# Kernel tuning notes

Hardware: AMD Instinct MI355X
Metric: run time of the kernel (lower is better)

Reference implementation:

```python
import jax, jax.numpy as jnp
import numpy as np

B_, L_, D_MODEL = 2, 4096, 1024
D_STATE, D_CONV, D_INNER = 64, 4, 2048
EPS = 1.1920929e-07  # torch.finfo(float32).eps, nn.RMSNorm default


def setup_inputs() -> dict:
    key = jax.random.key(0)
    ks = jax.random.split(key, 8)
    s = 0.02
    x = jax.random.normal(ks[0], (B_, L_, D_MODEL), jnp.float32)
    W_in = jax.random.normal(ks[1], (D_MODEL, 2 * D_INNER), jnp.float32) * s
    conv_w = jax.random.normal(ks[2], (D_INNER, 1, D_CONV), jnp.float32) * s  # depthwise (O,I/g,K)
    conv_b = jnp.zeros((D_INNER,), jnp.float32)
    W_x = jax.random.normal(ks[3], (D_INNER, 2 * D_STATE + D_INNER), jnp.float32) * s
    W_dt = jax.random.normal(ks[4], (D_INNER, D_INNER), jnp.float32) * s
    b_dt = jnp.zeros((D_INNER,), jnp.float32)
    A_log = jnp.log(jnp.tile(jnp.arange(1, D_STATE + 1, dtype=jnp.float32)[None, :], (D_INNER, 1)))
    D_param = jnp.ones((D_INNER,), jnp.float32)
    W_out = jax.random.normal(ks[5], (D_INNER, D_MODEL), jnp.float32) * s
    norm_w = jnp.ones((D_INNER,), jnp.float32)
    return dict(x=x, W_in=W_in, conv_w=conv_w, conv_b=conv_b, W_x=W_x, W_dt=W_dt,
                b_dt=b_dt, A_log=A_log, D_param=D_param, W_out=W_out, norm_w=norm_w)


def selective_scan(x_conv, dt, A, B_ssm, C_ssm, D_param):
    # x_conv,dt: (B,L,d_inner); A:(d_inner,d_state); B_ssm,C_ssm:(B,L,d_state)
    dt = jax.nn.softplus(dt)

    def step(h, inp):
        dt_t, B_t, C_t, x_t = inp  # (B,di),(B,ds),(B,ds),(B,di)
        dA = jnp.exp(dt_t[:, :, None] * A[None, :, :])           # (B,di,ds)
        h = dA * h + (dt_t * x_t)[:, :, None] * B_t[:, None, :]  # (B,di,ds)
        y = jnp.einsum('bds,bs->bd', h, C_t)                     # (B,di)
        return h, y

    h0 = jnp.zeros((x_conv.shape[0], A.shape[0], A.shape[1]), x_conv.dtype)
    xs = (jnp.moveaxis(dt, 1, 0), jnp.moveaxis(B_ssm, 1, 0),
          jnp.moveaxis(C_ssm, 1, 0), jnp.moveaxis(x_conv, 1, 0))
    _, ys = jax.lax.scan(step, h0, xs)
    y = jnp.moveaxis(ys, 0, 1)  # (B,L,d_inner)
    return y + x_conv * D_param[None, None, :]


def reference(x, W_in, conv_w, conv_b, W_x, W_dt, b_dt, A_log, D_param, W_out, norm_w):
    xz = x @ W_in                                    # (B,L,2*d_inner)
    x_ssm, z = jnp.split(xz, 2, axis=-1)
    # causal depthwise conv1d: left-pad d_conv-1 == torch pad-both-then-slice[:L]
    xc = jnp.swapaxes(x_ssm, 1, 2)                   # (B,d_inner,L)
    xc = jax.lax.conv_general_dilated(
        xc, conv_w, window_strides=(1,), padding=[(D_CONV - 1, 0)],
        dimension_numbers=('NCH', 'OIH', 'NCH'), feature_group_count=D_INNER)
    xc = xc + conv_b[None, :, None]
    xc = jax.nn.silu(jnp.swapaxes(xc, 1, 2))         # (B,L,d_inner)
    dbc = xc @ W_x                                   # (B,L,2*d_state+d_inner)
    B_ssm = dbc[..., :D_STATE]
    C_ssm = dbc[..., D_STATE:2 * D_STATE]
    dt = dbc[..., 2 * D_STATE:] @ W_dt + b_dt
    A = -jnp.exp(A_log)
    y = selective_scan(xc, dt, A, B_ssm, C_ssm, D_param)
    # RMSNorm then gate
    y = y * jax.lax.rsqrt(jnp.mean(y * y, axis=-1, keepdims=True) + EPS) * norm_w
    y = y * jax.nn.silu(z)
    return y @ W_out
```

## Files before the change

### kernel.cpp

```cpp
#include <hip/hip_runtime.h>
#include <hip/hip_bf16.h>

#define L_SEQ   4096
#define DMODEL  1024
#define DINNER  2048
#define DSTATE  64
#define NB      2
#define DPB     128
#define NROWS   (NB * L_SEQ)

typedef unsigned short u16;
typedef __attribute__((ext_vector_type(8))) short bf16x8;
typedef __attribute__((ext_vector_type(4))) float f32x4;

__device__ __forceinline__ float silu_f(float x)  { return x / (1.f + __expf(-x)); }
__device__ __forceinline__ float softplus_f(float x) {
    return x > 15.f ? x : __logf(1.f + __expf(x));
}
__device__ __forceinline__ float bf2f(u16 u) { return __uint_as_float(((unsigned)u) << 16); }
__device__ __forceinline__ u16 f2bf(float f) {
    __hip_bfloat16 h = __float2bfloat16(f);
    return *reinterpret_cast<u16*>(&h);
}
__device__ __forceinline__ unsigned pack2(float a, float b) {
    return (unsigned)f2bf(a) | ((unsigned)f2bf(b) << 16);
}

__global__ __launch_bounds__(256) void f32_to_bf16_kernel(
    const float* __restrict__ in, u16* __restrict__ out)
{
    const int i = (blockIdx.x * 256 + threadIdx.x) * 4;
    float4 v = *reinterpret_cast<const float4*>(in + i);
    ushort4 o;
    o.x = f2bf(v.x); o.y = f2bf(v.y); o.z = f2bf(v.z); o.w = f2bf(v.w);
    *reinterpret_cast<ushort4*>(out + i) = o;
}

__global__ __launch_bounds__(256) void transpose_bf16_kernel(
    const float* __restrict__ W, u16* __restrict__ Wt, int K, int N)
{
    __shared__ float t[32][33];
    const int n0 = blockIdx.x * 32, k0 = blockIdx.y * 32;
    const int tx = threadIdx.x & 31, ty = threadIdx.x >> 5;
    #pragma unroll
    for (int i = 0; i < 32; i += 8)
        t[ty + i][tx] = W[(size_t)(k0 + ty + i) * N + n0 + tx];
    __syncthreads();
    #pragma unroll
    for (int i = 0; i < 32; i += 8)
        Wt[(size_t)(n0 + ty + i) * K + k0 + tx] = f2bf(t[tx][ty + i]);
}

template <typename TC>
__global__ __launch_bounds__(256) void mfma_gemm(
    const u16* __restrict__ A, int lda,
    const u16* __restrict__ Bt, int ldb,
    TC* __restrict__ C, int ldc,
    int K, const float* __restrict__ bias)
{
    __shared__ u16 As[128 * 32];
    __shared__ u16 Bs[128 * 32];
    const int tid  = threadIdx.x;
    const int lane = tid & 63;
    const int w    = tid >> 6;
    const int wm   = w >> 1, wn = w & 1;

    const int gx = gridDim.x;
    const int nwg = gx * gridDim.y;
    int wg = blockIdx.y * gx + blockIdx.x;
    if ((nwg & 7) == 0) wg = (wg & 7) * (nwg >> 3) + (wg >> 3);
    const int bm = (wg / gx) * 128, bn = (wg % gx) * 128;

    const int lr = lane & 15, lk = lane >> 4;
    const int srow  = lane >> 2;
    const int scolb = (lane & 3) * 16;
    const size_t ldaB = (size_t)lda * 2, ldbB = (size_t)ldb * 2;

    const char* Ab = (const char*)A + (size_t)bm * ldaB;
    const char* Bb = (const char*)Bt + (size_t)bn * ldbB;
    char* AsB = (char*)As;
    char* BsB = (char*)Bs;

    f32x4 acc[4][4] = {};

    for (int k0 = 0; k0 < K; k0 += 32) {
        const size_t kb = (size_t)k0 * 2;
        #pragma unroll
        for (int i = 0; i < 2; ++i) {
            const int row = i * 64 + w * 16 + srow;
            __builtin_amdgcn_global_load_lds(
                (const __attribute__((address_space(1))) void*)(Ab + (size_t)row * ldaB + kb + scolb),
                (__attribute__((address_space(3))) void*)(AsB + i * 4096 + w * 1024),
                16, 0, 0);
            __builtin_amdgcn_global_load_lds(
                (const __attribute__((address_space(1))) void*)(Bb + (size_t)row * ldbB + kb + scolb),
                (__attribute__((address_space(3))) void*)(BsB + i * 4096 + w * 1024),
                16, 0, 0);
        }
        __syncthreads();
        bf16x8 a[4], b[4];
        #pragma unroll
        for (int mi = 0; mi < 4; ++mi)
            a[mi] = *reinterpret_cast<const bf16x8*>(&As[(wm * 64 + mi * 16 + lr) * 32 + lk * 8]);
        #pragma unroll
        for (int ni = 0; ni < 4; ++ni)
            b[ni] = *reinterpret_cast<const bf16x8*>(&Bs[(wn * 64 + ni * 16 + lr) * 32 + lk * 8]);
        #pragma unroll
        for (int mi = 0; mi < 4; ++mi)
            #pragma unroll
            for (int ni = 0; ni < 4; ++ni)
                acc[mi][ni] = __builtin_amdgcn_mfma_f32_16x16x32_bf16(a[mi], b[ni], acc[mi][ni], 0, 0, 0);
        __syncthreads();
    }

    float bv[4];
    if (bias) {
        #pragma unroll
        for (int ni = 0; ni < 4; ++ni) bv[ni] = bias[bn + wn * 64 + ni * 16 + lr];
    }
    #pragma unroll
    for (int mi = 0; mi < 4; ++mi) {
        #pragma unroll
        for (int ni = 0; ni < 4; ++ni) {
            #pragma unroll
            for (int r = 0; r < 4; ++r) {
                const int row = bm + wm * 64 + mi * 16 + lk * 4 + r;
                const int col = bn + wn * 64 + ni * 16 + lr;
                float v = acc[mi][ni][r];
                if (bias) v += bv[ni];
                if constexpr (sizeof(TC) == 4) C[(size_t)row * ldc + col] = v;
                else                           C[(size_t)row * ldc + col] = f2bf(v);
            }
        }
    }
}

#define BAR()  asm volatile("s_barrier" ::: "memory")
#define WV(n)  asm volatile("s_waitcnt vmcnt(" #n ")" ::: "memory")
#define STG16(s, d) __builtin_amdgcn_global_load_lds( \
    (const __attribute__((address_space(1))) void*)(s), \
    (__attribute__((address_space(3))) void*)(d), 16, 0, 0)

template <typename TC, int ACT>
__global__ __launch_bounds__(512, 2) void gemm256(
    const u16* __restrict__ A, int lda,
    const u16* __restrict__ Bt, int ldb,
    TC* __restrict__ C, int ldc,
    int K, const float* __restrict__ bias)
{
    extern __shared__ char lds[];
    const int tid = threadIdx.x;
    const int l = tid & 63, w = tid >> 6;
    const int wm = w >> 2, wn = w & 3;
    const int lr = l & 15, lk = l >> 4;

    const int gx = gridDim.x;
    const int nwg = gx * gridDim.y;
    int wg = blockIdx.y * gx + blockIdx.x;
    wg = (wg & 7) * (nwg >> 3) + (wg >> 3);
    const int bm = (wg / gx) * 256, bn = (wg % gx) * 256;

    const size_t ldaB = (size_t)lda * 2, ldbB = (size_t)ldb * 2;
    const int gsw = (((l & 7) ^ (l >> 3)) << 4);
    const char* aSrc = (const char*)A + (size_t)(bm + w * 8 + (l >> 3)) * ldaB + gsw;
    const char* bSrc = (const char*)Bt + (size_t)(bn + w * 8 + (l >> 3)) * ldbB + gsw;
    const int csw0 = (lk * 16) ^ ((lr & 7) << 4);
    const int wdst = w * 1024;

    const int nk = K >> 6;
    f32x4 acc[8][4] = {};

    {
        STG16(aSrc + (size_t)(0 * 64) * ldaB, lds + 0 * 8192 + wdst);
        STG16(aSrc + (size_t)(2 * 64) * ldaB, lds + 2 * 8192 + wdst);
        STG16(bSrc + (size_t)(0 * 64) * ldbB, lds + 32768 + 0 * 8192 + wdst);
        STG16(bSrc + (size_t)(1 * 64) * ldbB, lds + 32768 + 1 * 8192 + wdst);
        STG16(bSrc + (size_t)(2 * 64) * ldbB, lds + 32768 + 2 * 8192 + wdst);
        STG16(bSrc + (size_t)(3 * 64) * ldbB, lds + 32768 + 3 * 8192 + wdst);
        STG16(aSrc + (size_t)(1 * 64) * ldaB, lds + 1 * 8192 + wdst);
        STG16(aSrc + (size_t)(3 * 64) * ldaB, lds + 3 * 8192 + wdst);
        WV(2);
        BAR();
    }

    for (int t = 0; t < nk; ++t) {
        const int p = t & 1;
        const char* Ar = lds + (p << 16);
        const char* Br = Ar + 32768;
        const int tn = (t + 1 < nk) ? t + 1 : t;
        char* dq = lds + (((t + 1) & 1) << 16);
        const size_t Tb = (size_t)tn << 7;
        const char* aS = aSrc + Tb;
        const char* bS = bSrc + Tb;

        bf16x8 a[4][2], bf[2][2];

        #pragma unroll
        for (int mi = 0; mi < 4; ++mi) {
            const int ro = (wm * 128 + mi * 16 + lr) * 128;
            a[mi][0] = *reinterpret_cast<const bf16x8*>(Ar + ro + csw0);
            a[mi][1] = *reinterpret_cast<const bf16x8*>(Ar + ro + (csw0 ^ 64));
        }
        #pragma unroll
        for (int ni = 0; ni < 2; ++ni) {
            const int ro = (wn * 64 + ni * 16 + lr) * 128;
            bf[ni][0] = *reinterpret_cast<const bf16x8*>(Br + ro + csw0);
            bf[ni][1] = *reinterpret_cast<const bf16x8*>(Br + ro + (csw0 ^ 64));
        }
        STG16(aS + (size_t)(0 * 64) * ldaB, dq + 0 * 8192 + wdst);
        STG16(aS + (size_t)(2 * 64) * ldaB, dq + 2 * 8192 + wdst);
        BAR();
        __builtin_amdgcn_s_setprio(1);
        #pragma unroll
        for (int mi = 0; mi < 4; ++mi)
            #pragma unroll
            for (int ni = 0; ni < 2; ++ni) {
                acc[mi][ni] = __builtin_amdgcn_mfma_f32_16x16x32_bf16(a[mi][0], bf[ni][0], acc[mi][ni], 0, 0, 0);
                acc[mi][ni] = __builtin_amdgcn_mfma_f32_16x16x32_bf16(a[mi][1], bf[ni][1], acc[mi][ni], 0, 0, 0);
            }
        __builtin_amdgcn_s_setprio(0);
        BAR();

        #pragma unroll
        for (int ni = 0; ni < 2; ++ni) {
            const int ro = (wn * 64 + (2 + ni) * 16 + lr) * 128;
            bf[ni][0] = *reinterpret_cast<const bf16x8*>(Br + ro + csw0);
            bf[ni][1] = *reinterpret_cast<const bf16x8*>(Br + ro + (csw0 ^ 64));
        }
        STG16(bS + (size_t)(0 * 64) * ldbB, dq + 32768 + 0 * 8192 + wdst);
        STG16(bS + (size_t)(1 * 64) * ldbB, dq + 32768 + 1 * 8192 + wdst);
        BAR();
        __builtin_amdgcn_s_setprio(1);
        #pragma unroll
        for (int mi = 0; mi < 4; ++mi)
            #pragma unroll
            for (int ni = 0; ni < 2; ++ni) {
                acc[mi][2 + ni] = __builtin_amdgcn_mfma_f32_16x16x32_bf16(a[mi][0], bf[ni][0], acc[mi][2 + ni], 0, 0, 0);
                acc[mi][2 + ni] = __builtin_amdgcn_mfma_f32_16x16x32_bf16(a[mi][1], bf[ni][1], acc[mi][2 + ni], 0, 0, 0);
            }
        __builtin_amdgcn_s_setprio(0);
        WV(4);
        BAR();

        #pragma unroll
        for (int mi = 0; mi < 4; ++mi) {
            const int ro = (wm * 128 + (4 + mi) * 16 + lr) * 128;
            a[mi][0] = *reinterpret_cast<const bf16x8*>(Ar + ro + csw0);
            a[mi][1] = *reinterpret_cast<const bf16x8*>(Ar + ro + (csw0 ^ 64));
        }
        STG16(bS + (size_t)(2 * 64) * ldbB, dq + 32768 + 2 * 8192 + wdst);
        STG16(bS + (size_t)(3 * 64) * ldbB, dq + 32768 + 3 * 8192 + wdst);
        BAR();
        __builtin_amdgcn_s_setprio(1);
        #pragma unroll
        for (int mi = 0; mi < 4; ++mi)
            #pragma unroll
            for (int ni = 0; ni < 2; ++ni) {
                acc[4 + mi][2 + ni] = __builtin_amdgcn_mfma_f32_16x16x32_bf16(a[mi][0], bf[ni][0], acc[4 + mi][2 + ni], 0, 0, 0);
                acc[4 + mi][2 + ni] = __builtin_amdgcn_mfma_f32_16x16x32_bf16(a[mi][1], bf[ni][1], acc[4 + mi][2 + ni], 0, 0, 0);
            }
        __builtin_amdgcn_s_setprio(0);
        BAR();

        #pragma unroll
        for (int ni = 0; ni < 2; ++ni) {
            const int ro = (wn * 64 + ni * 16 + lr) * 128;
            bf[ni][0] = *reinterpret_cast<const bf16x8*>(Br + ro + csw0);
            bf[ni][1] = *reinterpret_cast<const bf16x8*>(Br + ro + (csw0 ^ 64));
        }
        STG16(aS + (size_t)(1 * 64) * ldaB, dq + 1 * 8192 + wdst);
        STG16(aS + (size_t)(3 * 64) * ldaB, dq + 3 * 8192 + wdst);
        BAR();
        __builtin_amdgcn_s_setprio(1);
        #pragma unroll
        for (int mi = 0; mi < 4; ++mi)
            #pragma unroll
            for (int ni = 0; ni < 2; ++ni) {
                acc[4 + mi][ni] = __builtin_amdgcn_mfma_f32_16x16x32_bf16(a[mi][0], bf[ni][0], acc[4 + mi][ni], 0, 0, 0);
                acc[4 + mi][ni] = __builtin_amdgcn_mfma_f32_16x16x32_bf16(a[mi][1], bf[ni][1], acc[4 + mi][ni], 0, 0, 0);
            }
        __builtin_amdgcn_s_setprio(0);
        WV(2);
        BAR();
    }

    float bv[4];
    if (bias) {
        #pragma unroll
        for (int ni = 0; ni < 4; ++ni) bv[ni] = bias[bn + wn * 64 + ni * 16 + lr];
    }
    #pragma unroll
    for (int mi = 0; mi < 8; ++mi) {
        #pragma unroll
        for (int ni = 0; ni < 4; ++ni) {
            #pragma unroll
            for (int r = 0; r < 4; ++r) {
                const int row = bm + wm * 128 + mi * 16 + lk * 4 + r;
                const int col = bn + wn * 64 + ni * 16 + lr;
                float v = acc[mi][ni][r];
                if (bias) v += bv[ni];
                if constexpr (ACT == 1) v = softplus_f(v);
                if constexpr (sizeof(TC) == 4) C[(size_t)row * ldc + col] = v;
                else                           C[(size_t)row * ldc + col] = f2bf(v);
            }
        }
    }
}

__global__ __launch_bounds__(256) void conv_silu_kernel(
    const u16* __restrict__ xz, const float* __restrict__ cw,
    const float* __restrict__ cb, u16* __restrict__ xc)
{
    const int idx8 = blockIdx.x * 256 + threadIdx.x;
    const int db  = (idx8 & 255) << 3;
    const int row = idx8 >> 8;
    const int l   = row & (L_SEQ - 1);

    float v[4][8];
    #pragma unroll
    for (int k = 0; k < 4; ++k) {
        const int ll = l - 3 + k;
        if (ll >= 0) {
            uint4 u = *reinterpret_cast<const uint4*>(xz + (size_t)(row - 3 + k) * 4096 + db);
            v[k][0]=bf2f((u16)(u.x&0xffff)); v[k][1]=bf2f((u16)(u.x>>16));
            v[k][2]=bf2f((u16)(u.y&0xffff)); v[k][3]=bf2f((u16)(u.y>>16));
            v[k][4]=bf2f((u16)(u.z&0xffff)); v[k][5]=bf2f((u16)(u.z>>16));
            v[k][6]=bf2f((u16)(u.w&0xffff)); v[k][7]=bf2f((u16)(u.w>>16));
        } else {
            #pragma unroll
            for (int j = 0; j < 8; ++j) v[k][j] = 0.f;
        }
    }
    float acc[8];
    {
        float4 c0 = *reinterpret_cast<const float4*>(cb + db);
        float4 c1 = *reinterpret_cast<const float4*>(cb + db + 4);
        acc[0]=c0.x; acc[1]=c0.y; acc[2]=c0.z; acc[3]=c0.w;
        acc[4]=c1.x; acc[5]=c1.y; acc[6]=c1.z; acc[7]=c1.w;
    }
    #pragma unroll
    for (int j = 0; j < 8; ++j) {
        const float4 wv = reinterpret_cast<const float4*>(cw)[db + j];
        acc[j] = fmaf(v[0][j], wv.x, acc[j]);
        acc[j] = fmaf(v[1][j], wv.y, acc[j]);
        acc[j] = fmaf(v[2][j], wv.z, acc[j]);
        acc[j] = fmaf(v[3][j], wv.w, acc[j]);
    }
    uint4 o;
    o.x = pack2(silu_f(acc[0]), silu_f(acc[1]));
    o.y = pack2(silu_f(acc[2]), silu_f(acc[3]));
    o.z = pack2(silu_f(acc[4]), silu_f(acc[5]));
    o.w = pack2(silu_f(acc[6]), silu_f(acc[7]));
    *reinterpret_cast<uint4*>(xc + (size_t)row * 2048 + db) = o;
}


__device__ __forceinline__ int a_pattern_check_half(
    const float* A_log, int d, int base, float& A0)
{
    A0 = -__expf(A_log[d * DSTATE]);
    int ok = 1;
    #pragma unroll
    for (int j = 0; j < 32; ++j) {
        const int s = base + j;
        const float As = -__expf(A_log[d * DSTATE + s]);
        ok &= (fabsf(As - A0 * (float)(s + 1)) <= 1e-3f * (float)(s + 1));
    }
    return ok;
}

#define UNPACK8(dstp, u)  do {                                             \
    float4 _a, _b;                                                         \
    _a.x=bf2f((u16)((u).x&0xffff)); _a.y=bf2f((u16)((u).x>>16));           \
    _a.z=bf2f((u16)((u).y&0xffff)); _a.w=bf2f((u16)((u).y>>16));           \
    _b.x=bf2f((u16)((u).z&0xffff)); _b.y=bf2f((u16)((u).z>>16));           \
    _b.z=bf2f((u16)((u).w&0xffff)); _b.w=bf2f((u16)((u).w>>16));           \
    *reinterpret_cast<float4*>(dstp) = _a;                                 \
    *reinterpret_cast<float4*>((dstp) + 4) = _b;                           \
} while (0)

__global__ __launch_bounds__(256) void scan_phase1(
    const u16* __restrict__ xc,
    const u16* __restrict__ dbc,
    const float* __restrict__ A_log,
    float* __restrict__ hend, float* __restrict__ sumdt,
    int nchunk, int chunk)
{
    const int tid  = threadIdx.x;
    const int dl   = tid >> 1, half = tid & 1;
    const int base = half * 32;
    const int d0   = blockIdx.x * DPB;
    const int d    = d0 + dl;
    const int c = blockIdx.y, b = blockIdx.z;
    const int t0 = c * chunk;
    const size_t bL = (size_t)b * L_SEQ;

    __shared__ float dts_s[16][132];
    __shared__ float xcs_s[16][132];
    __shared__ float Bs_s[16][68];

    float A0;
    int fast = a_pattern_check_half(A_log, d, base, A0);
    fast = __syncthreads_and(fast);

    float h[32];
    #pragma unroll
    for (int j = 0; j < 32; ++j) h[j] = 0.f;
    float sd = 0.f;

    for (int ts = 0; ts < chunk; ts += 16) {
        __syncthreads();
        {
            const int rr = tid >> 4, cc = (tid & 15) * 8;
            const size_t row = bL + t0 + ts + rr;
            uint4 v = *reinterpret_cast<const uint4*>(dbc + row * 2176 + 128 + d0 + cc);
            UNPACK8(&dts_s[rr][cc], v);
            uint4 u = *reinterpret_cast<const uint4*>(xc + row * 2048 + d0 + cc);
            UNPACK8(&xcs_s[rr][cc], u);
        }
        if (tid < 128) {
            const int rr = tid >> 3, cc = (tid & 7) * 8;
            const size_t row = bL + t0 + ts + rr;
            uint4 v = *reinterpret_cast<const uint4*>(dbc + row * 2176 + cc);
            UNPACK8(&Bs_s[rr][cc], v);
        }
        __syncthreads();
        if (fast) {
            for (int r = 0; r < 16; ++r) {
                const float dts = dts_s[r][dl];
                const float xv  = xcs_s[r][dl];
                const float dtx = dts * xv;
                sd += dts;
                const float q  = __expf(A0 * dts);
                const float q2 = q * q, q4 = q2 * q2;
                const float q8 = q4 * q4, q16 = q8 * q8, q32 = q16 * q16;
                const float qb = half ? q32 : 1.f;
                float p0 = qb * q, p1 = qb * q2, p2 = p1 * q, p3 = qb * q4;
                #pragma unroll
                for (int g = 0; g < 8; ++g) {
                    const float4 Bv = *reinterpret_cast<const float4*>(&Bs_s[r][base + g * 4]);
                    h[g*4+0] = fmaf(p0, h[g*4+0], dtx * Bv.x);
                    h[g*4+1] = fmaf(p1, h[g*4+1], dtx * Bv.y);
                    h[g*4+2] = fmaf(p2, h[g*4+2], dtx * Bv.z);
                    h[g*4+3] = fmaf(p3, h[g*4+3], dtx * Bv.w);
                    p0 *= q4; p1 *= q4; p2 *= q4; p3 *= q4;
                }
            }
        } else {
            for (int r = 0; r < 16; ++r) {
                const float dts = dts_s[r][dl];
                const float xv  = xcs_s[r][dl];
                const float dtx = dts * xv;
                sd += dts;
                #pragma unroll
                for (int j = 0; j < 32; ++j) {
                    const float a = __expf(-__expf(A_log[d * DSTATE + base + j]) * dts);
                    h[j] = fmaf(a, h[j], dtx * Bs_s[r][base + j]);
                }
            }
        }
    }
    const size_t cb64 = ((size_t)b * nchunk + c) * DSTATE;
    #pragma unroll
    for (int j = 0; j < 32; ++j) hend[(cb64 + base + j) * DINNER + d] = h[j];
    if (half == 0) sumdt[((size_t)b * nchunk + c) * DINNER + d] = sd;
}

__global__ __launch_bounds__(256) void scan_phase2(
    float* __restrict__ hbuf, const float* __restrict__ sumdt,
    const float* __restrict__ A_log, int nchunk)
{
    const int idx = blockIdx.x * 256 + threadIdx.x;
    const int d = idx & (DINNER - 1);
    const int s = (idx >> 11) & (DSTATE - 1);
    const int b = idx >> 17;

    const float A = -__expf(A_log[d * DSTATE + s]);
    float h = 0.f;
    for (int c = 0; c < nchunk; ++c) {
        const size_t off = (((size_t)b * nchunk + c) * DSTATE + s) * DINNER + d;
        const float he = hbuf[off];
        const float ap = __expf(A * sumdt[((size_t)b * nchunk + c) * DINNER + d]);
        hbuf[off] = h;
        h = fmaf(ap, h, he);
    }
}

__global__ __launch_bounds__(256) void scan_phase3(
    u16* __restrict__ xc,
    const u16* __restrict__ dbc,
    const float* __restrict__ A_log,
    const float* __restrict__ hinit,
    const float* __restrict__ D_param,
    int nchunk, int chunk)
{
    const int tid  = threadIdx.x;
    const int dl   = tid >> 1, half = tid & 1;
    const int base = half * 32;
    const int d0   = blockIdx.x * DPB;
    const int d    = d0 + dl;
    const int c = blockIdx.y, b = blockIdx.z;
    const int t0 = c * chunk;
    const size_t bL = (size_t)b * L_SEQ;

    __shared__ float dts_s[16][132];
    __shared__ float xcs_s[16][132];
    __shared__ float BCs[16][132];

    float A0;
    int fast = a_pattern_check_half(A_log, d, base, A0);
    fast = __syncthreads_and(fast);

    float h[32];
    {
        const size_t cb64 = ((size_t)b * nchunk + c) * DSTATE;
        #pragma unroll
        for (int j = 0; j < 32; ++j) h[j] = hinit[(cb64 + base + j) * DINNER + d];
    }
    const float Dp = D_param[d];

    for (int ts = 0; ts < chunk; ts += 16) {
        __syncthreads();
        {
            const int rr = tid >> 4, cc = (tid & 15) * 8;
            const size_t row = bL + t0 + ts + rr;
            uint4 v = *reinterpret_cast<const uint4*>(dbc + row * 2176 + 128 + d0 + cc);
            UNPACK8(&dts_s[rr][cc], v);
            uint4 u = *reinterpret_cast<const uint4*>(xc + row * 2048 + d0 + cc);
            UNPACK8(&xcs_s[rr][cc], u);
            uint4 w = *reinterpret_cast<const uint4*>(dbc + row * 2176 + cc);
            UNPACK8(&BCs[rr][cc], w);
        }
        __syncthreads();
        if (fast) {
            for (int r = 0; r < 16; ++r) {
                const float dts = dts_s[r][dl];
                const float xv  = xcs_s[r][dl];
                const float dtx = dts * xv;
                const float q  = __expf(A0 * dts);
                const float q2 = q * q, q4 = q2 * q2;
                const float q8 = q4 * q4, q16 = q8 * q8, q32 = q16 * q16;
                const float qb = half ? q32 : 1.f;
                float p0 = qb * q, p1 = qb * q2, p2 = p1 * q, p3 = qb * q4;
                float y = 0.f;
                #pragma unroll
                for (int g = 0; g < 8; ++g) {
                    const float4 Bv = *reinterpret_cast<const float4*>(&BCs[r][base + g * 4]);
                    const float4 Cv = *reinterpret_cast<const float4*>(&BCs[r][64 + base + g * 4]);
                    h[g*4+0] = fmaf(p0, h[g*4+0], dtx * Bv.x);  y = fmaf(h[g*4+0], Cv.x, y);
                    h[g*4+1] = fmaf(p1, h[g*4+1], dtx * Bv.y);  y = fmaf(h[g*4+1], Cv.y, y);
                    h[g*4+2] = fmaf(p2, h[g*4+2], dtx * Bv.z);  y = fmaf(h[g*4+2], Cv.z, y);
                    h[g*4+3] = fmaf(p3, h[g*4+3], dtx * Bv.w);  y = fmaf(h[g*4+3], Cv.w, y);
                    p0 *= q4; p1 *= q4; p2 *= q4; p3 *= q4;
                }
                const float yt = y + __shfl_xor(y, 1, 64);
                if (half == 0) {
                    const size_t row = bL + t0 + ts + r;
                    xc[row * 2048 + d] = f2bf(fmaf(xv, Dp, yt));
                }
            }
        } else {
            for (int r = 0; r < 16; ++r) {
                const float dts = dts_s[r][dl];
                const float xv  = xcs_s[r][dl];
                const float dtx = dts * xv;
                float y = 0.f;
                #pragma unroll
                for (int j = 0; j < 32; ++j) {
                    const float a = __expf(-__expf(A_log[d * DSTATE + base + j]) * dts);
                    h[j] = fmaf(a, h[j], dtx * BCs[r][base + j]);
                    y = fmaf(h[j], BCs[r][64 + base + j], y);
                }
                const float yt = y + __shfl_xor(y, 1, 64);
                if (half == 0) {
                    const size_t row = bL + t0 + ts + r;
                    xc[row * 2048 + d] = f2bf(fmaf(xv, Dp, yt));
                }
            }
        }
    }
}

__global__ __launch_bounds__(256) void rms_gate_kernel(
    u16* __restrict__ y, const u16* __restrict__ xz,
    const float* __restrict__ norm_w)
{
    const int row = blockIdx.x;
    const int tid = threadIdx.x;
    const size_t ybase = (size_t)row * DINNER;
    const size_t zbase = (size_t)row * 4096 + DINNER;
    const int i8 = tid * 8;

    float yv[8];
    {
        uint4 u = *reinterpret_cast<const uint4*>(y + ybase + i8);
        yv[0]=bf2f((u16)(u.x&0xffff)); yv[1]=bf2f((u16)(u.x>>16));
        yv[2]=bf2f((u16)(u.y&0xffff)); yv[3]=bf2f((u16)(u.y>>16));
        yv[4]=bf2f((u16)(u.z&0xffff)); yv[5]=bf2f((u16)(u.z>>16));
        yv[6]=bf2f((u16)(u.w&0xffff)); yv[7]=bf2f((u16)(u.w>>16));
    }
    float ss = 0.f;
    #pragma unroll
    for (int j = 0; j < 8; ++j) ss = fmaf(yv[j], yv[j], ss);
    #pragma unroll
    for (int off = 32; off > 0; off >>= 1) ss += __shfl_down(ss, off, 64);
    __shared__ float sred[4];
    const int lane = tid & 63, wid = tid >> 6;
    if (lane == 0) sred[wid] = ss;
    __syncthreads();
    const float tot = sred[0] + sred[1] + sred[2] + sred[3];
    const float scale = rsqrtf(tot * (1.f / (float)DINNER) + 1.1920929e-07f);

    float zv[8];
    {
        uint4 u = *reinterpret_cast<const uint4*>(xz + zbase + i8);
        zv[0]=bf2f((u16)(u.x&0xffff)); zv[1]=bf2f((u16)(u.x>>16));
        zv[2]=bf2f((u16)(u.y&0xffff)); zv[3]=bf2f((u16)(u.y>>16));
        zv[4]=bf2f((u16)(u.z&0xffff)); zv[5]=bf2f((u16)(u.z>>16));
        zv[6]=bf2f((u16)(u.w&0xffff)); zv[7]=bf2f((u16)(u.w>>16));
    }
    float4 n0 = *reinterpret_cast<const float4*>(norm_w + i8);
    float4 n1 = *reinterpret_cast<const float4*>(norm_w + i8 + 4);
    const float nw[8] = {n0.x,n0.y,n0.z,n0.w,n1.x,n1.y,n1.z,n1.w};
    float o[8];
    #pragma unroll
    for (int j = 0; j < 8; ++j) o[j] = yv[j] * scale * nw[j] * silu_f(zv[j]);
    uint4 ov;
    ov.x = pack2(o[0], o[1]); ov.y = pack2(o[2], o[3]);
    ov.z = pack2(o[4], o[5]); ov.w = pack2(o[6], o[7]);
    *reinterpret_cast<uint4*>(y + ybase + i8) = ov;
}

extern "C" void kernel_launch(void* const* d_in, const int* in_sizes, int n_in,
                              void* d_out, int out_size, void* d_ws, size_t ws_size,
                              hipStream_t stream)
{
    const float* x       = (const float*)d_in[0];
    const float* W_in    = (const float*)d_in[1];
    const float* conv_w  = (const float*)d_in[2];
    const float* conv_b  = (const float*)d_in[3];
    const float* W_x     = (const float*)d_in[4];
    const float* W_dt    = (const float*)d_in[5];
    const float* b_dt    = (const float*)d_in[6];
    const float* A_log   = (const float*)d_in[7];
    const float* D_param = (const float*)d_in[8];
    const float* W_out   = (const float*)d_in[9];
    const float* norm_w  = (const float*)d_in[10];
    float* out = (float*)d_out;

    hipFuncSetAttribute(reinterpret_cast<const void*>(&gemm256<u16, 0>),
                        hipFuncAttributeMaxDynamicSharedMemorySize, 131072);
    hipFuncSetAttribute(reinterpret_cast<const void*>(&gemm256<u16, 1>),
                        hipFuncAttributeMaxDynamicSharedMemorySize, 131072);

    char* ws = (char*)d_ws;
    u16* xz  = (u16*)(ws);
    u16* xc  = (u16*)(ws + 67108864ull);
    u16* dbc = (u16*)(ws + 100663296ull);
    u16* xbf  = dbc;
    u16* Wxbf = xz;
    u16* Wt_out = (u16*)(ws + 136314880ull);
    const size_t fixed_bytes = 140509184ull;
    const size_t per_chunk = 2ull * DSTATE * DINNER * 4 + 2ull * DINNER * 4;
    int nchunk = 64;
    while (nchunk > 1 && fixed_bytes + (size_t)nchunk * per_chunk > ws_size) nchunk >>= 1;
    const int chunk = L_SEQ / nchunk;
    float* hbuf = (float*)(ws + fixed_bytes);
    float* sdt  = (float*)(ws + fixed_bytes + (size_t)nchunk * 2ull * DSTATE * DINNER * 4);

    u16* Wt_in = (u16*)d_out;
    u16* Wt_x  = Wt_in + 4194304ull;
    u16* Wt_dt = Wt_x + 4456448ull;

    const int M = NROWS;

    f32_to_bf16_kernel<<<(M * DMODEL) / 1024, 256, 0, stream>>>(x, xbf);
    f32_to_bf16_kernel<<<(DINNER * 2176) / 1024, 256, 0, stream>>>(W_x, Wxbf);
    transpose_bf16_kernel<<<dim3(4096 / 32, 1024 / 32), 256, 0, stream>>>(W_in, Wt_in, 1024, 4096);
    transpose_bf16_kernel<<<dim3(4, 2048 / 32), 256, 0, stream>>>(W_x, Wt_x, 2048, 2176);
    transpose_bf16_kernel<<<dim3(2048 / 32, 2048 / 32), 256, 0, stream>>>(W_dt, Wt_dt, 2048, 2048);
    transpose_bf16_kernel<<<dim3(1024 / 32, 2048 / 32), 256, 0, stream>>>(W_out, Wt_out, 2048, 1024);
    mfma_gemm<u16><<<dim3(2048 / 128, 2048 / 128), 256, 0, stream>>>(
        Wt_dt, 2048, Wxbf + 128, 2176, Wt_x + 128ull * 2048, 2048, 2048, nullptr);

    gemm256<u16, 0><<<dim3(4096 / 256, M / 256), 512, 131072, stream>>>(
        xbf, DMODEL, Wt_in, DMODEL, xz, 4096, DMODEL, nullptr);
    conv_silu_kernel<<<(M * DINNER) / (256 * 8), 256, 0, stream>>>(xz, conv_w, conv_b, xc);
    mfma_gemm<u16><<<dim3(1, M / 128), 256, 0, stream>>>(
        xc, DINNER, Wt_x, DINNER, dbc, 2176, DINNER, nullptr);
    gemm256<u16, 1><<<dim3(2048 / 256, M / 256), 512, 131072, stream>>>(
        xc, DINNER, Wt_x + 128ull * 2048, DINNER, dbc + 128, 2176, DINNER, b_dt);
    scan_phase1<<<dim3(DINNER / DPB, nchunk, NB), 256, 0, stream>>>(
        xc, dbc, A_log, hbuf, sdt, nchunk, chunk);
    scan_phase2<<<(NB * DINNER * DSTATE) / 256, 256, 0, stream>>>(hbuf, sdt, A_log, nchunk);
    scan_phase3<<<dim3(DINNER / DPB, nchunk, NB), 256, 0, stream>>>(
        xc, dbc, A_log, hbuf, D_param, nchunk, chunk);
    rms_gate_kernel<<<M, 256, 0, stream>>>(xc, xz, norm_w);
    mfma_gemm<float><<<dim3(1024 / 128, M / 128), 256, 0, stream>>>(
        xc, DINNER, Wt_out, DINNER, out, DMODEL, DINNER, nullptr);
}
```

Measured before the change: 653.3 us.

## Merge B/C projection and dt GEMMs into one padded GEMM; pack scan math

The separate small mfma_gemm for the B/C columns and the gemm256 for dt (with softplus) become a single gemm256 over a 2304-wide output. The weight matrix is zero-padded from 2176 to 2304 columns, and a concatenated bias is applied, with softplus only on columns ≥128. This removes one launch and the poorly parallel 1-column-block GEMM, at the cost of computing 128 wasted padded columns. The scan phases also switch to float2 vector arithmetic, which may let the compiler emit packed FP32 instructions.

Result: no change. 654.0 us (+0.1%).

```diff
diff --git a/kernel.cpp b/kernel.cpp
--- a/kernel.cpp
+++ b/kernel.cpp
@@ -7,11 +7,13 @@
 #define DSTATE  64
 #define NB      2
 #define DPB     128
+#define DBCS    2304
 #define NROWS   (NB * L_SEQ)
 
 typedef unsigned short u16;
 typedef __attribute__((ext_vector_type(8))) short bf16x8;
 typedef __attribute__((ext_vector_type(4))) float f32x4;
+typedef __attribute__((ext_vector_type(2))) float f32x2;
 
 __device__ __forceinline__ float silu_f(float x)  { return x / (1.f + __expf(-x)); }
 __device__ __forceinline__ float softplus_f(float x) {
@@ -49,6 +51,15 @@
     #pragma unroll
     for (int i = 0; i < 32; i += 8)
         Wt[(size_t)(n0 + ty + i) * K + k0 + tx] = f2bf(t[tx][ty + i]);
+}
+
+__global__ __launch_bounds__(256) void bias_cat_kernel(
+    const float* __restrict__ b_dt, float* __restrict__ bias)
+{
+    const int i = blockIdx.x * 256 + threadIdx.x;
+    float v = 0.f;
+    if (i >= 128 && i < 128 + DINNER) v = b_dt[i - 128];
+    bias[i] = v;
 }
 
 template <typename TC>
@@ -299,7 +310,7 @@
                 const int col = bn + wn * 64 + ni * 16 + lr;
                 float v = acc[mi][ni][r];
                 if (bias) v += bv[ni];
-                if constexpr (ACT == 1) v = softplus_f(v);
+                if constexpr (ACT == 2) { if (col >= 128) v = softplus_f(v); }
                 if constexpr (sizeof(TC) == 4) C[(size_t)row * ldc + col] = v;
                 else                           C[(size_t)row * ldc + col] = f2bf(v);
             }
@@ -403,9 +414,9 @@
     int fast = a_pattern_check_half(A_log, d, base, A0);
     fast = __syncthreads_and(fast);
 
-    float h[32];
-    #pragma unroll
-    for (int j = 0; j < 32; ++j) h[j] = 0.f;
+    f32x2 h2[16];
+    #pragma unroll
+    for (int j = 0; j < 16; ++j) h2[j] = (f32x2){0.f, 0.f};
     float sd = 0.f;
 
     for (int ts = 0; ts < chunk; ts += 16) {
@@ -413,7 +424,7 @@
         {
             const int rr = tid >> 4, cc = (tid & 15) * 8;
             const size_t row = bL + t0 + ts + rr;
-            uint4 v = *reinterpret_cast<const uint4*>(dbc + row * 2176 + 128 + d0 + cc);
+            uint4 v = *reinterpret_cast<const uint4*>(dbc + row * DBCS + 128 + d0 + cc);
             UNPACK8(&dts_s[rr][cc], v);
             uint4 u = *reinterpret_cast<const uint4*>(xc + row * 2048 + d0 + cc);
             UNPACK8(&xcs_s[rr][cc], u);
@@ -421,7 +432,7 @@
         if (tid < 128) {
             const int rr = tid >> 3, cc = (tid & 7) * 8;
             const size_t row = bL + t0 + ts + rr;
-            uint4 v = *reinterpret_cast<const uint4*>(dbc + row * 2176 + cc);
+            uint4 v = *reinterpret_cast<const uint4*>(dbc + row * DBCS + cc);
             UNPACK8(&Bs_s[rr][cc], v);
         }
         __syncthreads();
@@ -432,21 +443,24 @@
                 const float dtx = dts * xv;
                 sd += dts;
                 const float q  = __expf(A0 * dts);
-                const float q2 = q * q, q4 = q2 * q2;
+                const float q2 = q * q, q3 = q2 * q, q4 = q2 * q2;
                 const float q8 = q4 * q4, q16 = q8 * q8, q32 = q16 * q16;
                 const float qb = half ? q32 : 1.f;
-                float p0 = qb * q, p1 = qb * q2, p2 = p1 * q, p3 = qb * q4;
+                f32x2 pA = {qb * q, qb * q2};
+                f32x2 pB = {qb * q3, qb * q4};
+                const f32x2 q44 = {q4, q4};
+                const f32x2 dtx2 = {dtx, dtx};
                 #pragma unroll
                 for (int g = 0; g < 8; ++g) {
-                    const float4 Bv = *reinterpret_cast<const float4*>(&Bs_s[r][base + g * 4]);
-                    h[g*4+0] = fmaf(p0, h[g*4+0], dtx * Bv.x);
-                    h[g*4+1] = fmaf(p1, h[g*4+1], dtx * Bv.y);
-                    h[g*4+2] = fmaf(p2, h[g*4+2], dtx * Bv.z);
-                    h[g*4+3] = fmaf(p3, h[g*4+3], dtx * Bv.w);
-                    p0 *= q4; p1 *= q4; p2 *= q4; p3 *= q4;
+                    const f32x2 B01 = *reinterpret_cast<const f32x2*>(&Bs_s[r][base + g * 4]);
+                    const f32x2 B23 = *reinterpret_cast<const f32x2*>(&Bs_s[r][base + g * 4 + 2]);
+                    h2[2*g]   = pA * h2[2*g]   + B01 * dtx2;
+                    h2[2*g+1] = pB * h2[2*g+1] + B23 * dtx2;
+                    pA = pA * q44; pB = pB * q44;
                 }
             }
         } else {
+            float* hs = (float*)h2;
             for (int r = 0; r < 16; ++r) {
                 const float dts = dts_s[r][dl];
                 const float xv  = xcs_s[r][dl];
@@ -455,14 +469,15 @@
                 #pragma unroll
                 for (int j = 0; j < 32; ++j) {
                     const float a = __expf(-__expf(A_log[d * DSTATE + base + j]) * dts);
-                    h[j] = fmaf(a, h[j], dtx * Bs_s[r][base + j]);
+                    hs[j] = fmaf(a, hs[j], dtx * Bs_s[r][base + j]);
                 }
             }
         }
     }
     const size_t cb64 = ((size_t)b * nchunk + c) * DSTATE;
-    #pragma unroll
-    for (int j = 0; j < 32; ++j) hend[(cb64 + base + j) * DINNER + d] = h[j];
+    const float* hs = (const float*)h2;
+    #pragma unroll
+    for (int j = 0; j < 32; ++j) hend[(cb64 + base + j) * DINNER + d] = hs[j];
     if (half == 0) sumdt[((size_t)b * nchunk + c) * DINNER + d] = sd;
 }
 
@@ -511,11 +526,12 @@
     int fast = a_pattern_check_half(A_log, d, base, A0);
     fast = __syncthreads_and(fast);
 
-    float h[32];
+    f32x2 h2[16];
     {
         const size_t cb64 = ((size_t)b * nchunk + c) * DSTATE;
-        #pragma unroll
-        for (int j = 0; j < 32; ++j) h[j] = hinit[(cb64 + base + j) * DINNER + d];
+        float* hs = (float*)h2;
+        #pragma unroll
+        for (int j = 0; j < 32; ++j) hs[j] = hinit[(cb64 + base + j) * DINNER + d];
     }
     const float Dp = D_param[d];
 
@@ -524,11 +540,11 @@
         {
             const int rr = tid >> 4, cc = (tid & 15) * 8;
             const size_t row = bL + t0 + ts + rr;
-            uint4 v = *reinterpret_cast<const uint4*>(dbc + row * 2176 + 128 + d0 + cc);
+            uint4 v = *reinterpret_cast<const uint4*>(dbc + row * DBCS + 128 + d0 + cc);
             UNPACK8(&dts_s[rr][cc], v);
             uint4 u = *reinterpret_cast<const uint4*>(xc + row * 2048 + d0 + cc);
             UNPACK8(&xcs_s[rr][cc], u);
-            uint4 w = *reinterpret_cast<const uint4*>(dbc + row * 2176 + cc);
+            uint4 w = *reinterpret_cast<const uint4*>(dbc + row * DBCS + cc);
             UNPACK8(&BCs[rr][cc], w);
         }
         __syncthreads();
@@ -538,21 +554,27 @@
                 const float xv  = xcs_s[r][dl];
                 const float dtx = dts * xv;
                 const float q  = __expf(A0 * dts);
-                const float q2 = q * q, q4 = q2 * q2;
+                const float q2 = q * q, q3 = q2 * q, q4 = q2 * q2;
                 const float q8 = q4 * q4, q16 = q8 * q8, q32 = q16 * q16;
                 const float qb = half ? q32 : 1.f;
-                float p0 = qb * q, p1 = qb * q2, p2 = p1 * q, p3 = qb * q4;
-                float y = 0.f;
+                f32x2 pA = {qb * q, qb * q2};
+                f32x2 pB = {qb * q3, qb * q4};
+                const f32x2 q44 = {q4, q4};
+                const f32x2 dtx2 = {dtx, dtx};
+                f32x2 y2 = {0.f, 0.f};
                 #pragma unroll
                 for (int g = 0; g < 8; ++g) {
-                    const float4 Bv = *reinterpret_cast<const float4*>(&BCs[r][base + g * 4]);
-                    const float4 Cv = *reinterpret_cast<const float4*>(&BCs[r][64 + base + g * 4]);
-                    h[g*4+0] = fmaf(p0, h[g*4+0], dtx * Bv.x);  y = fmaf(h[g*4+0], Cv.x, y);
-                    h[g*4+1] = fmaf(p1, h[g*4+1], dtx * Bv.y);  y = fmaf(h[g*4+1], Cv.y, y);
-                    h[g*4+2] = fmaf(p2, h[g*4+2], dtx * Bv.z);  y = fmaf(h[g*4+2], Cv.z, y);
-                    h[g*4+3] = fmaf(p3, h[g*4+3], dtx * Bv.w);  y = fmaf(h[g*4+3], Cv.w, y);
-                    p0 *= q4; p1 *= q4; p2 *= q4; p3 *= q4;
+                    const f32x2 B01 = *reinterpret_cast<const f32x2*>(&BCs[r][base + g * 4]);
+                    const f32x2 B23 = *reinterpret_cast<const f32x2*>(&BCs[r][base + g * 4 + 2]);
+                    const f32x2 C01 = *reinterpret_cast<const f32x2*>(&BCs[r][64 + base + g * 4]);
+                    const f32x2 C23 = *reinterpret_cast<const f32x2*>(&BCs[r][64 + base + g * 4 + 2]);
+                    h2[2*g]   = pA * h2[2*g]   + B01 * dtx2;
+                    h2[2*g+1] = pB * h2[2*g+1] + B23 * dtx2;
+                    y2 = h2[2*g] * C01 + y2;
+                    y2 = h2[2*g+1] * C23 + y2;
+                    pA = pA * q44; pB = pB * q44;
                 }
+                float y = y2.x + y2.y;
                 const float yt = y + __shfl_xor(y, 1, 64);
                 if (half == 0) {
                     const size_t row = bL + t0 + ts + r;
@@ -560,6 +582,7 @@
                 }
             }
         } else {
+            float* hs = (float*)h2;
             for (int r = 0; r < 16; ++r) {
                 const float dts = dts_s[r][dl];
                 const float xv  = xcs_s[r][dl];
@@ -568,8 +591,8 @@
                 #pragma unroll
                 for (int j = 0; j < 32; ++j) {
                     const float a = __expf(-__expf(A_log[d * DSTATE + base + j]) * dts);
-                    h[j] = fmaf(a, h[j], dtx * BCs[r][base + j]);
-                    y = fmaf(h[j], BCs[r][64 + base + j], y);
+                    hs[j] = fmaf(a, hs[j], dtx * BCs[r][base + j]);
+                    y = fmaf(hs[j], BCs[r][64 + base + j], y);
                 }
                 const float yt = y + __shfl_xor(y, 1, 64);
                 if (half == 0) {
@@ -650,7 +673,7 @@
 
     hipFuncSetAttribute(reinterpret_cast<const void*>(&gemm256<u16, 0>),
                         hipFuncAttributeMaxDynamicSharedMemorySize, 131072);
-    hipFuncSetAttribute(reinterpret_cast<const void*>(&gemm256<u16, 1>),
+    hipFuncSetAttribute(reinterpret_cast<const void*>(&gemm256<u16, 2>),
                         hipFuncAttributeMaxDynamicSharedMemorySize, 131072);
 
     char* ws = (char*)d_ws;
@@ -659,8 +682,9 @@
     u16* dbc = (u16*)(ws + 100663296ull);
     u16* xbf  = dbc;
     u16* Wxbf = xz;
-    u16* Wt_out = (u16*)(ws + 136314880ull);
-    const size_t fixed_bytes = 140509184ull;
+    u16* Wt_out = (u16*)(ws + 138412032ull);
+    float* bias2304 = (float*)(ws + 142606336ull);
+    const size_t fixed_bytes = 142615552ull;
     const size_t per_chunk = 2ull * DSTATE * DINNER * 4 + 2ull * DINNER * 4;
     int nchunk = 64;
     while (nchunk > 1 && fixed_bytes + (size_t)nchunk * per_chunk > ws_size) nchunk >>= 1;
@@ -670,7 +694,7 @@
 
     u16* Wt_in = (u16*)d_out;
     u16* Wt_x  = Wt_in + 4194304ull;
-    u16* Wt_dt = Wt_x + 4456448ull;
+    u16* Wt_dt = Wt_x + 4718592ull;
 
     const int M = NROWS;
 
@@ -680,16 +704,16 @@
     transpose_bf16_kernel<<<dim3(4, 2048 / 32), 256, 0, stream>>>(W_x, Wt_x, 2048, 2176);
     transpose_bf16_kernel<<<dim3(2048 / 32, 2048 / 32), 256, 0, stream>>>(W_dt, Wt_dt, 2048, 2048);
     transpose_bf16_kernel<<<dim3(1024 / 32, 2048 / 32), 256, 0, stream>>>(W_out, Wt_out, 2048, 1024);
+    bias_cat_kernel<<<9, 256, 0, stream>>>(b_dt, bias2304);
+    hipMemsetAsync(Wt_x + 2176ull * 2048, 0, 128ull * 2048 * 2, stream);
     mfma_gemm<u16><<<dim3(2048 / 128, 2048 / 128), 256, 0, stream>>>(
         Wt_dt, 2048, Wxbf + 128, 2176, Wt_x + 128ull * 2048, 2048, 2048, nullptr);
 
     gemm256<u16, 0><<<dim3(4096 / 256, M / 256), 512, 131072, stream>>>(
         xbf, DMODEL, Wt_in, DMODEL, xz, 4096, DMODEL, nullptr);
     conv_silu_kernel<<<(M * DINNER) / (256 * 8), 256, 0, stream>>>(xz, conv_w, conv_b, xc);
-    mfma_gemm<u16><<<dim3(1, M / 128), 256, 0, stream>>>(
-        xc, DINNER, Wt_x, DINNER, dbc, 2176, DINNER, nullptr);
-    gemm256<u16, 1><<<dim3(2048 / 256, M / 256), 512, 131072, stream>>>(
-        xc, DINNER, Wt_x + 128ull * 2048, DINNER, dbc + 128, 2176, DINNER, b_dt);
+    gemm256<u16, 2><<<dim3(DBCS / 256, M / 256), 512, 131072, stream>>>(
+        xc, DINNER, Wt_x, DINNER, dbc, DBCS, DINNER, bias2304);
     scan_phase1<<<dim3(DINNER / DPB, nchunk, NB), 256, 0, stream>>>(
         xc, dbc, A_log, hbuf, sdt, nchunk, chunk);
     scan_phase2<<<(NB * DINNER * DSTATE) / 256, 256, 0, stream>>>(hbuf, sdt, A_log, nchunk);
```
